# Kernel tuning notes

Hardware: AMD Instinct MI355X
Metric: run time of the kernel (lower is better)

Reference implementation:

```python
import jax, jax.numpy as jnp
import numpy as np

N = 100000
NEG_SLOPE = 0.2
ALPHA = 0.5


def _glorot(key, shape):
    fan_in, fan_out = shape[0], shape[-1]
    lim = jnp.sqrt(6.0 / (fan_in + fan_out))
    return jax.random.uniform(key, shape, jnp.float32, -lim, lim)


def setup_inputs() -> dict:
    key = jax.random.key(0)
    ks = jax.random.split(key, 16)
    x = jax.random.normal(ks[0], (N, 512), jnp.float32)
    spatial_edge_index = jax.random.randint(ks[1], (2, 800000), 0, N, jnp.int64)
    gene_sim_edge_index = jax.random.randint(ks[2], (2, 800000), 0, N, jnp.int64)
    # spatial GAT params (in=512 -> hid=256)
    W_sp = _glorot(ks[3], (512, 256)); a_src_sp = _glorot(ks[4], (256,)); a_dst_sp = _glorot(ks[5], (256,)); b_sp = jnp.zeros((256,), jnp.float32)
    # gene-sim GAT params
    W_gs = _glorot(ks[6], (512, 256)); a_src_gs = _glorot(ks[7], (256,)); a_dst_gs = _glorot(ks[8], (256,)); b_gs = jnp.zeros((256,), jnp.float32)
    # fusion GAT params (hid=256 -> out=64)
    W_fu = _glorot(ks[9], (256, 64)); a_src_fu = _glorot(ks[10], (64,)); a_dst_fu = _glorot(ks[11], (64,)); b_fu = jnp.zeros((64,), jnp.float32)
    return {"x": x, "spatial_edge_index": spatial_edge_index, "gene_sim_edge_index": gene_sim_edge_index,
            "W_sp": W_sp, "a_src_sp": a_src_sp, "a_dst_sp": a_dst_sp, "b_sp": b_sp,
            "W_gs": W_gs, "a_src_gs": a_src_gs, "a_dst_gs": a_dst_gs, "b_gs": b_gs,
            "W_fu": W_fu, "a_src_fu": a_src_fu, "a_dst_fu": a_dst_fu, "b_fu": b_fu}


def gat_conv(x, edge_index, W, a_src, a_dst, bias):
    """PyG GATConv, heads=1, concat=False, add_self_loops=True."""
    n = x.shape[0]
    h = x @ W  # [N, H]
    loops = jnp.arange(n, dtype=edge_index.dtype)
    src = jnp.concatenate([edge_index[0], loops])  # message source j
    dst = jnp.concatenate([edge_index[1], loops])  # aggregation target i
    e = jax.nn.leaky_relu((h @ a_src)[src] + (h @ a_dst)[dst], NEG_SLOPE)  # [E+N]
    # segment softmax over incoming edges of each dst node
    m = jax.ops.segment_max(e, dst, num_segments=n)
    ex = jnp.exp(e - m[dst])
    denom = jax.ops.segment_sum(ex, dst, num_segments=n)
    coef = ex / denom[dst]
    out = jax.ops.segment_sum(coef[:, None] * h[src], dst, num_segments=n)
    return out + bias


def reference(x, spatial_edge_index, gene_sim_edge_index,
              W_sp, a_src_sp, a_dst_sp, b_sp,
              W_gs, a_src_gs, a_dst_gs, b_gs,
              W_fu, a_src_fu, a_dst_fu, b_fu):
    h_spatial = jax.nn.elu(gat_conv(x, spatial_edge_index, W_sp, a_src_sp, a_dst_sp, b_sp))
    h_gene = jax.nn.elu(gat_conv(x, gene_sim_edge_index, W_gs, a_src_gs, a_dst_gs, b_gs))
    h_fused = ALPHA * h_gene + (1.0 - ALPHA) * h_spatial
    return gat_conv(h_fused, spatial_edge_index, W_fu, a_src_fu, a_dst_fu, b_fu)
```

## Files before the change

### kernel.cpp

```cpp
#include <hip/hip_runtime.h>
#include <math.h>


#define NEG_SLOPE 0.2f

typedef __attribute__((ext_vector_type(8))) short bf16x8;
typedef __attribute__((ext_vector_type(4))) float f32x4;
typedef __attribute__((ext_vector_type(2))) float f32x2;

__device__ __forceinline__ unsigned short f2bf(float f) {
  unsigned int u = __float_as_uint(f);
  u = (u + 0x7FFFu + ((u >> 16) & 1u)) >> 16;
  return (unsigned short)u;
}
__device__ __forceinline__ float bf2f(unsigned short u) {
  return __uint_as_float((unsigned int)u << 16);
}
__device__ __forceinline__ f32x2 unpk(unsigned int u) {
  f32x2 r;
  r.x = __uint_as_float(u << 16);
  r.y = __uint_as_float(u & 0xFFFF0000u);
  return r;
}
__device__ __forceinline__ int rl_i(int v, int l) {
  return __builtin_amdgcn_readlane(v, l);
}
__device__ __forceinline__ float rl_f(float v, int l) {
  return __uint_as_float(__builtin_amdgcn_readlane(__float_as_uint(v), l));
}

#define GLOAD16(g, l)                                                   \
  __builtin_amdgcn_global_load_lds(                                     \
      (const __attribute__((address_space(1))) void*)(g),               \
      (__attribute__((address_space(3))) void*)(l), 16, 0, 0)

__global__ __launch_bounds__(256) void wt_bf16_all(const float* __restrict__ W_sp,
                                                   const float* __restrict__ W_gs,
                                                   const float* __restrict__ W_fu,
                                                   unsigned short* __restrict__ wt_sp,
                                                   unsigned short* __restrict__ wt_gs,
                                                   unsigned short* __restrict__ wt_fu) {
  const int i = blockIdx.x * 256 + threadIdx.x;
  if (i < 131072) {
    const int k = i >> 8, n = i & 255;
    wt_sp[n * 512 + k] = f2bf(W_sp[i]);
  } else if (i < 262144) {
    const int j = i - 131072;
    const int k = j >> 8, n = j & 255;
    wt_gs[n * 512 + k] = f2bf(W_gs[j]);
  } else if (i < 278528) {
    const int j = i - 262144;
    const int k = j >> 6, n = j & 63;
    wt_fu[n * 256 + k] = f2bf(W_fu[j]);
  }
}

__global__ __launch_bounds__(256) void hist2(const int* __restrict__ dst_sp,
                                             const int* __restrict__ dst_gs,
                                             int* __restrict__ deg_sp,
                                             int* __restrict__ deg_gs,
                                             int* __restrict__ ord_sp,
                                             int* __restrict__ ord_gs, int E) {
  const int m = blockIdx.x * 256 + threadIdx.x;
  if (m < E) {
    ord_sp[m] = atomicAdd(&deg_sp[dst_sp[m]], 1);
    ord_gs[m] = atomicAdd(&deg_gs[dst_gs[m]], 1);
  }
}

__global__ __launch_bounds__(256) void scan1_2(const int* __restrict__ deg_sp,
                                               const int* __restrict__ deg_gs,
                                               int* __restrict__ rs_sp,
                                               int* __restrict__ rs_gs,
                                               int* __restrict__ parts2, int N) {
  __shared__ int sm[256];
  const int* deg = blockIdx.y ? deg_gs : deg_sp;
  int* rs = blockIdx.y ? rs_gs : rs_sp;
  int* parts = parts2 + blockIdx.y * 512;
  const int i = blockIdx.x * 256 + threadIdx.x;
  const int v = (i < N) ? deg[i] : 0;
  sm[threadIdx.x] = v;
  __syncthreads();
  for (int off = 1; off < 256; off <<= 1) {
    const int x = (threadIdx.x >= off) ? sm[threadIdx.x - off] : 0;
    __syncthreads();
    sm[threadIdx.x] += x;
    __syncthreads();
  }
  if (i < N) rs[i] = sm[threadIdx.x] - v;
  if (threadIdx.x == 255) parts[blockIdx.x] = sm[255];
}

__global__ __launch_bounds__(512) void scan2_2(int* __restrict__ parts2, int nb) {
  __shared__ int sm[512];
  int* parts = parts2 + blockIdx.x * 512;
  const int t = threadIdx.x;
  const int v = (t < nb) ? parts[t] : 0;
  sm[t] = v;
  __syncthreads();
  for (int off = 1; off < 512; off <<= 1) {
    const int x = (t >= off) ? sm[t - off] : 0;
    __syncthreads();
    sm[t] += x;
    __syncthreads();
  }
  if (t < nb) parts[t] = sm[t] - v;
}

__global__ __launch_bounds__(256) void scan3_2(int* __restrict__ rs_sp,
                                               int* __restrict__ rs_gs,
                                               const int* __restrict__ parts2,
                                               int N, int E) {
  int* rs = blockIdx.y ? rs_gs : rs_sp;
  const int* parts = parts2 + blockIdx.y * 512;
  const int i = blockIdx.x * 256 + threadIdx.x;
  if (i < N) rs[i] += parts[blockIdx.x];
  if (i == 0) rs[N] = E;
}

__global__ __launch_bounds__(256) void scatter2(const int* __restrict__ ei_sp,
                                                const int* __restrict__ ei_gs,
                                                const int* __restrict__ rs_sp,
                                                const int* __restrict__ rs_gs,
                                                const int* __restrict__ ord_sp,
                                                const int* __restrict__ ord_gs,
                                                int* __restrict__ csr_sp,
                                                int* __restrict__ csr_gs, int E) {
  const int m = blockIdx.x * 256 + threadIdx.x;
  if (m >= E) return;
  csr_sp[rs_sp[ei_sp[E + m]] + ord_sp[m]] = ei_sp[m];
  csr_gs[rs_gs[ei_gs[E + m]] + ord_gs[m]] = ei_gs[m];
}

__global__ __launch_bounds__(512) void gemm2_fused(const float* __restrict__ x,
                                                   const unsigned short* __restrict__ wsp,
                                                   const unsigned short* __restrict__ wgs,
                                                   unsigned short* __restrict__ hb_sp,
                                                   unsigned short* __restrict__ hb_gs,
                                                   int M) {
  __shared__ unsigned short sA[64 * 64];
  __shared__ unsigned short sW[2][256 * 64];
  const int tid = threadIdx.x;
  const int w = tid >> 6, l = tid & 63;
  const int whalf = w >> 2;
  const int wq = w & 3;
  const int bm = blockIdx.x * 64;

  const int arow0 = tid >> 4;
  const int acol4 = (tid & 15) * 4;
  const unsigned short* __restrict__ wtp = whalf ? wgs : wsp;
  const int wrow_in_ch = l >> 3;
  const int wbyte = ((l & 7) * 16) ^ ((wrow_in_ch & 7) << 4);

  f32x4 acc[4][4] = {};
  for (int k0 = 0; k0 < 512; k0 += 64) {
    __syncthreads();
#pragma unroll
    for (int r = 0; r < 2; ++r) {
      const int row = arow0 + r * 32;
      int grow = bm + row;
      grow = grow < M ? grow : M - 1;
      const float4 v = *(const float4*)(x + (size_t)grow * 512 + k0 + acol4);
      ushort4 o;
      o.x = f2bf(v.x); o.y = f2bf(v.y); o.z = f2bf(v.z); o.w = f2bf(v.w);
      const int byte = (row * 128 + acol4 * 2) ^ ((row & 7) << 4);
      *(ushort4*)(((char*)sA) + byte) = o;
    }
#pragma unroll
    for (int c = 0; c < 8; ++c) {
      const int ch = c * 4 + wq;
      const int grow = ch * 8 + wrow_in_ch;
      const char* g = (const char*)wtp + (size_t)grow * 1024 + (size_t)k0 * 2 + wbyte;
      GLOAD16(g, ((char*)sW[whalf]) + ch * 1024);
    }
    __syncthreads();
#pragma unroll
    for (int ks = 0; ks < 2; ++ks) {
      const int cb = ks * 64 + (l >> 4) * 16;
      bf16x8 af[4], bf[4];
#pragma unroll
      for (int m = 0; m < 4; ++m) {
        const int r = m * 16 + (l & 15);
        af[m] = *(const bf16x8*)(((const char*)sA) + r * 128 + (cb ^ ((r & 7) << 4)));
      }
#pragma unroll
      for (int n = 0; n < 4; ++n) {
        const int r = wq * 64 + n * 16 + (l & 15);
        bf[n] = *(const bf16x8*)(((const char*)sW[whalf]) + r * 128 + (cb ^ ((r & 7) << 4)));
      }
#pragma unroll
      for (int m = 0; m < 4; ++m)
#pragma unroll
        for (int n = 0; n < 4; ++n)
          acc[m][n] = __builtin_amdgcn_mfma_f32_16x16x32_bf16(af[m], bf[n], acc[m][n], 0, 0, 0);
    }
  }
  unsigned short* __restrict__ outp = whalf ? hb_gs : hb_sp;
#pragma unroll
  for (int m = 0; m < 4; ++m) {
#pragma unroll
    for (int r = 0; r < 4; ++r) {
      const int row = bm + m * 16 + (l >> 4) * 4 + r;
      if (row < M) {
#pragma unroll
        for (int n = 0; n < 4; ++n)
          outp[(size_t)row * 256 + wq * 64 + n * 16 + (l & 15)] = f2bf(acc[m][n][r]);
      }
    }
  }
}

__global__ __launch_bounds__(256) void alpha2_256(const ushort4* __restrict__ hsp,
                                                  const ushort4* __restrict__ hgs,
                                                  const float* __restrict__ av_sp_s,
                                                  const float* __restrict__ av_sp_d,
                                                  const float* __restrict__ av_gs_s,
                                                  const float* __restrict__ av_gs_d,
                                                  float* __restrict__ asrc_sp,
                                                  float* __restrict__ adst_sp,
                                                  float* __restrict__ asrc_gs,
                                                  float* __restrict__ adst_gs, int N) {
  const int wave = (int)((blockIdx.x * (size_t)blockDim.x + threadIdx.x) >> 6);
  const int lane = threadIdx.x & 63;
  if (wave >= N) return;
  const ushort4 h1 = hsp[(size_t)wave * 64 + lane];
  const ushort4 h2 = hgs[(size_t)wave * 64 + lane];
  const float4 s1 = ((const float4*)av_sp_s)[lane];
  const float4 d1 = ((const float4*)av_sp_d)[lane];
  const float4 s2 = ((const float4*)av_gs_s)[lane];
  const float4 d2 = ((const float4*)av_gs_d)[lane];
  const float a0 = bf2f(h1.x), a1 = bf2f(h1.y), a2 = bf2f(h1.z), a3 = bf2f(h1.w);
  const float b0 = bf2f(h2.x), b1 = bf2f(h2.y), b2 = bf2f(h2.z), b3 = bf2f(h2.w);
  float p0 = a0 * s1.x + a1 * s1.y + a2 * s1.z + a3 * s1.w;
  float p1 = a0 * d1.x + a1 * d1.y + a2 * d1.z + a3 * d1.w;
  float p2 = b0 * s2.x + b1 * s2.y + b2 * s2.z + b3 * s2.w;
  float p3 = b0 * d2.x + b1 * d2.y + b2 * d2.z + b3 * d2.w;
#pragma unroll
  for (int off = 32; off; off >>= 1) {
    p0 += __shfl_down(p0, off);
    p1 += __shfl_down(p1, off);
    p2 += __shfl_down(p2, off);
    p3 += __shfl_down(p3, off);
  }
  if (lane == 0) {
    asrc_sp[wave] = p0; adst_sp[wave] = p1;
    asrc_gs[wave] = p2; adst_gs[wave] = p3;
  }
}

__global__ __launch_bounds__(256) void gemm_fu_alpha(const unsigned short* __restrict__ A,
                                                     const unsigned short* __restrict__ Bt,
                                                     const float* __restrict__ avs,
                                                     const float* __restrict__ avd,
                                                     unsigned short* __restrict__ C,
                                                     float* __restrict__ asrc,
                                                     float* __restrict__ adst,
                                                     int M) {
  constexpr int K = 256, Nc = 64;
  __shared__ unsigned short sA[128 * 64];
  __shared__ unsigned short sB[64 * 64];
  const int tid = threadIdx.x;
  const int w = tid >> 6, l = tid & 63;
  const int bm = blockIdx.x * 128;
  const int crow = l >> 3;
  const int cbyte = (l & 7) * 16;

  f32x4 acc[2][4] = {};
  for (int k0 = 0; k0 < K; k0 += 64) {
    __syncthreads();
#pragma unroll
    for (int c = 0; c < 4; ++c) {
      const int ch = w * 4 + c;
      int row = bm + ch * 8 + crow;
      row = row < M ? row : M - 1;
      const char* g = (const char*)A + (size_t)row * K * 2 + (size_t)k0 * 2 + cbyte;
      GLOAD16(g, ((char*)sA) + ch * 1024);
    }
#pragma unroll
    for (int c = 0; c < 2; ++c) {
      const int ch = w * 2 + c;
      const int row = ch * 8 + crow;
      const char* g = (const char*)Bt + (size_t)row * K * 2 + (size_t)k0 * 2 + cbyte;
      GLOAD16(g, ((char*)sB) + ch * 1024);
    }
    __syncthreads();
#pragma unroll
    for (int ks = 0; ks < 2; ++ks) {
      bf16x8 af[2], bfr[4];
#pragma unroll
      for (int m = 0; m < 2; ++m) {
        const int r = w * 32 + m * 16 + (l & 15);
        af[m] = *(const bf16x8*)&sA[r * 64 + ks * 32 + (l >> 4) * 8];
      }
#pragma unroll
      for (int n = 0; n < 4; ++n) {
        const int r = n * 16 + (l & 15);
        bfr[n] = *(const bf16x8*)&sB[r * 64 + ks * 32 + (l >> 4) * 8];
      }
#pragma unroll
      for (int m = 0; m < 2; ++m)
#pragma unroll
        for (int n = 0; n < 4; ++n)
          acc[m][n] = __builtin_amdgcn_mfma_f32_16x16x32_bf16(af[m], bfr[n], acc[m][n], 0, 0, 0);
    }
  }
  float as_v[4], ad_v[4];
#pragma unroll
  for (int n = 0; n < 4; ++n) {
    as_v[n] = avs[n * 16 + (l & 15)];
    ad_v[n] = avd[n * 16 + (l & 15)];
  }
#pragma unroll
  for (int m = 0; m < 2; ++m) {
#pragma unroll
    for (int r = 0; r < 4; ++r) {
      const int row = bm + w * 32 + m * 16 + (l >> 4) * 4 + r;
      if (row < M) {
#pragma unroll
        for (int n = 0; n < 4; ++n)
          C[(size_t)row * Nc + n * 16 + (l & 15)] = f2bf(acc[m][n][r]);
      }
      float ps = acc[m][0][r] * as_v[0] + acc[m][1][r] * as_v[1] +
                 acc[m][2][r] * as_v[2] + acc[m][3][r] * as_v[3];
      float pd = acc[m][0][r] * ad_v[0] + acc[m][1][r] * ad_v[1] +
                 acc[m][2][r] * ad_v[2] + acc[m][3][r] * ad_v[3];
#pragma unroll
      for (int off = 1; off < 16; off <<= 1) {
        ps += __shfl_xor(ps, off);
        pd += __shfl_xor(pd, off);
      }
      if ((l & 15) == 0 && row < M) {
        asrc[row] = ps;
        adst[row] = pd;
      }
    }
  }
}

__global__ __launch_bounds__(256) void agg2_blend(const int* __restrict__ rs_sp,
                                                  const int* __restrict__ csr_sp,
                                                  const int* __restrict__ rs_gs,
                                                  const int* __restrict__ csr_gs,
                                                  const float* __restrict__ asrc_sp,
                                                  const float* __restrict__ adst_sp,
                                                  const float* __restrict__ asrc_gs,
                                                  const float* __restrict__ adst_gs,
                                                  const uint2* __restrict__ hsp4,
                                                  const uint2* __restrict__ hgs4,
                                                  const float* __restrict__ b_sp,
                                                  const float* __restrict__ b_gs,
                                                  ushort4* __restrict__ out16, int N) {
  const int d = (int)((blockIdx.x * (size_t)blockDim.x + threadIdx.x) >> 6);
  const int lane = threadIdx.x & 63;
  if (d >= N) return;

  float v_sp[4], v_gs[4];
#pragma unroll
  for (int g = 0; g < 2; ++g) {
    const int* __restrict__ rs   = g ? rs_gs : rs_sp;
    const int* __restrict__ csr  = g ? csr_gs : csr_sp;
    const float* __restrict__ as = g ? asrc_gs : asrc_sp;
    const float* __restrict__ adp = g ? adst_gs : adst_sp;
    const uint2* __restrict__ h4 = g ? hgs4 : hsp4;
    const float* __restrict__ bias = g ? b_gs : b_sp;
    float* __restrict__ vout = g ? v_gs : v_sp;

    const float ad = adp[d];
    float e = as[d] + ad;
    e = e > 0.f ? e : NEG_SLOPE * e;
    const float wself = expf(e);
    float denl = (lane == 0) ? wself : 0.f;
    const uint2 hv = h4[(size_t)d * 64 + lane];
    f32x2 axy = unpk(hv.x) * wself;
    f32x2 azw = unpk(hv.y) * wself;

    const int base = rs[d], mend = rs[d + 1];
    for (int c = base; c < mend; c += 64) {
      const int m = c + lane;
      int s = 0;
      float w = 0.f;
      if (m < mend) {
        s = csr[m];
        float e2 = as[s] + ad;
        e2 = e2 > 0.f ? e2 : NEG_SLOPE * e2;
        w = expf(e2);
      }
      denl += w;
      const int cnt = min(64, mend - c);
      int j = 0;
      for (; j + 3 < cnt; j += 4) {
        const int s0 = rl_i(s, j), s1 = rl_i(s, j + 1), s2 = rl_i(s, j + 2), s3 = rl_i(s, j + 3);
        const float w0 = rl_f(w, j), w1 = rl_f(w, j + 1), w2 = rl_f(w, j + 2), w3 = rl_f(w, j + 3);
        const uint2 a0 = h4[(size_t)s0 * 64 + lane];
        const uint2 a1 = h4[(size_t)s1 * 64 + lane];
        const uint2 a2 = h4[(size_t)s2 * 64 + lane];
        const uint2 a3 = h4[(size_t)s3 * 64 + lane];
        axy += unpk(a0.x) * w0;  azw += unpk(a0.y) * w0;
        axy += unpk(a1.x) * w1;  azw += unpk(a1.y) * w1;
        axy += unpk(a2.x) * w2;  azw += unpk(a2.y) * w2;
        axy += unpk(a3.x) * w3;  azw += unpk(a3.y) * w3;
      }
      for (; j < cnt; ++j) {
        const int sj = rl_i(s, j);
        const float wj = rl_f(w, j);
        const uint2 aj = h4[(size_t)sj * 64 + lane];
        axy += unpk(aj.x) * wj;
        azw += unpk(aj.y) * wj;
      }
    }
#pragma unroll
    for (int off = 32; off; off >>= 1) denl += __shfl_xor(denl, off);
    const float inv = 1.f / denl;
    const float4 b4 = ((const float4*)bias)[lane];
    vout[0] = axy.x * inv + b4.x;
    vout[1] = axy.y * inv + b4.y;
    vout[2] = azw.x * inv + b4.z;
    vout[3] = azw.y * inv + b4.w;
#pragma unroll
    for (int j2 = 0; j2 < 4; ++j2)
      vout[j2] = vout[j2] > 0.f ? vout[j2] : (expf(vout[j2]) - 1.f);
  }

  ushort4 pk;
  pk.x = f2bf(0.5f * v_gs[0] + 0.5f * v_sp[0]);
  pk.y = f2bf(0.5f * v_gs[1] + 0.5f * v_sp[1]);
  pk.z = f2bf(0.5f * v_gs[2] + 0.5f * v_sp[2]);
  pk.w = f2bf(0.5f * v_gs[3] + 0.5f * v_sp[3]);
  out16[(size_t)d * 64 + lane] = pk;
}

__global__ __launch_bounds__(256) void agg_csr64(const int* __restrict__ rs,
                                                 const int* __restrict__ csr,
                                                 const float* __restrict__ asrc,
                                                 const float* __restrict__ adst,
                                                 const unsigned short* __restrict__ h,
                                                 const float* __restrict__ bias,
                                                 float* __restrict__ outb, int N) {
  const int d = (int)((blockIdx.x * (size_t)blockDim.x + threadIdx.x) >> 6);
  const int lane = threadIdx.x & 63;
  if (d >= N) return;
  const float ad = adst[d];

  float e = asrc[d] + ad;
  e = e > 0.f ? e : NEG_SLOPE * e;
  const float wself = expf(e);
  float denl = (lane == 0) ? wself : 0.f;
  f32x2 acc2;
  acc2.x = wself * bf2f(h[(size_t)d * 64 + lane]);
  acc2.y = 0.f;

  const int base = rs[d], mend = rs[d + 1];
  for (int c = base; c < mend; c += 64) {
    const int m = c + lane;
    int s = 0;
    float w = 0.f;
    if (m < mend) {
      s = csr[m];
      float e2 = asrc[s] + ad;
      e2 = e2 > 0.f ? e2 : NEG_SLOPE * e2;
      w = expf(e2);
    }
    denl += w;
    const int cnt = min(64, mend - c);
    int j = 0;
    for (; j + 3 < cnt; j += 4) {
      const int s0 = rl_i(s, j), s1 = rl_i(s, j + 1), s2 = rl_i(s, j + 2), s3 = rl_i(s, j + 3);
      const float w0 = rl_f(w, j), w1 = rl_f(w, j + 1), w2 = rl_f(w, j + 2), w3 = rl_f(w, j + 3);
      f32x2 h01, h23, w01, w23;
      h01.x = bf2f(h[(size_t)s0 * 64 + lane]);
      h01.y = bf2f(h[(size_t)s1 * 64 + lane]);
      h23.x = bf2f(h[(size_t)s2 * 64 + lane]);
      h23.y = bf2f(h[(size_t)s3 * 64 + lane]);
      w01.x = w0; w01.y = w1;
      w23.x = w2; w23.y = w3;
      acc2 += h01 * w01;
      acc2 += h23 * w23;
    }
    for (; j < cnt; ++j) {
      const int sj = rl_i(s, j);
      const float wj = rl_f(w, j);
      acc2.x += wj * bf2f(h[(size_t)sj * 64 + lane]);
    }
  }
  float acc = acc2.x + acc2.y;
#pragma unroll
  for (int off = 32; off; off >>= 1) denl += __shfl_xor(denl, off);
  outb[(size_t)d * 64 + lane] = acc / denl + bias[lane];
}

extern "C" void kernel_launch(void* const* d_in, const int* in_sizes, int n_in,
                              void* d_out, int out_size, void* d_ws, size_t ws_size,
                              hipStream_t stream) {
  const float* x        = (const float*)d_in[0];
  const int*   ei_sp    = (const int*)d_in[1];
  const int*   ei_gs    = (const int*)d_in[2];
  const float* W_sp     = (const float*)d_in[3];
  const float* a_src_sp = (const float*)d_in[4];
  const float* a_dst_sp = (const float*)d_in[5];
  const float* b_sp     = (const float*)d_in[6];
  const float* W_gs     = (const float*)d_in[7];
  const float* a_src_gs = (const float*)d_in[8];
  const float* a_dst_gs = (const float*)d_in[9];
  const float* b_gs     = (const float*)d_in[10];
  const float* W_fu     = (const float*)d_in[11];
  const float* a_src_fu = (const float*)d_in[12];
  const float* a_dst_fu = (const float*)d_in[13];
  const float* b_fu     = (const float*)d_in[14];
  float* out = (float*)d_out;

  const int N = in_sizes[0] / 512;
  const int E = in_sizes[1] / 2;
  const int nb = (N + 255) / 256;

  unsigned short* wt_sp = (unsigned short*)d_ws;
  unsigned short* wt_gs = wt_sp + 256 * 512;
  unsigned short* wt_fu = wt_gs + 256 * 512;
  unsigned short* hb_sp = wt_fu + 64 * 256;
  unsigned short* hb_gs = hb_sp + (size_t)N * 256;
  unsigned short* hfb   = hb_gs + (size_t)N * 256;
  unsigned short* hfu   = hfb + (size_t)N * 256;
  float* asrc_sp = (float*)(hfu + (size_t)N * 64);
  float* adst_sp = asrc_sp + N;
  float* asrc_gs = adst_sp + N;
  float* adst_gs = asrc_gs + N;
  int* rs_sp  = (int*)(adst_gs + N);
  int* rs_gs  = rs_sp + (N + 1);
  int* csr_sp = rs_gs + (N + 1);
  int* csr_gs = csr_sp + E;
  int* deg_sp = csr_gs + E;
  int* deg_gs = deg_sp + N;
  int* parts2 = deg_gs + N;
  int* ord_sp = parts2 + 1024;
  int* ord_gs = ord_sp + E;

  const int BLK = 256;
  const int eGrid = (E + BLK - 1) / BLK;
  const int nodeWaveGrid = (N + 3) / 4;

  hipMemsetAsync(deg_sp, 0, (size_t)2 * N * 4, stream);
  hist2<<<eGrid, BLK, 0, stream>>>(ei_sp + E, ei_gs + E, deg_sp, deg_gs,
                                   ord_sp, ord_gs, E);
  scan1_2<<<dim3(nb, 2), BLK, 0, stream>>>(deg_sp, deg_gs, rs_sp, rs_gs, parts2, N);
  scan2_2<<<2, 512, 0, stream>>>(parts2, nb);
  scan3_2<<<dim3(nb, 2), BLK, 0, stream>>>(rs_sp, rs_gs, parts2, N, E);
  scatter2<<<eGrid, BLK, 0, stream>>>(ei_sp, ei_gs, rs_sp, rs_gs, ord_sp, ord_gs,
                                      csr_sp, csr_gs, E);

  wt_bf16_all<<<(278528 + 255) / 256, BLK, 0, stream>>>(W_sp, W_gs, W_fu,
                                                        wt_sp, wt_gs, wt_fu);

  gemm2_fused<<<(N + 63) / 64, 512, 0, stream>>>(x, wt_sp, wt_gs, hb_sp, hb_gs, N);

  alpha2_256<<<nodeWaveGrid, BLK, 0, stream>>>((const ushort4*)hb_sp,
                                               (const ushort4*)hb_gs,
                                               a_src_sp, a_dst_sp, a_src_gs, a_dst_gs,
                                               asrc_sp, adst_sp, asrc_gs, adst_gs, N);

  agg2_blend<<<nodeWaveGrid, BLK, 0, stream>>>(rs_sp, csr_sp, rs_gs, csr_gs,
                                               asrc_sp, adst_sp, asrc_gs, adst_gs,
                                               (const uint2*)hb_sp,
                                               (const uint2*)hb_gs,
                                               b_sp, b_gs, (ushort4*)hfb, N);

  gemm_fu_alpha<<<(N + 127) / 128, BLK, 0, stream>>>(hfb, wt_fu, a_src_fu, a_dst_fu,
                                                     hfu, asrc_sp, adst_sp, N);
  agg_csr64<<<nodeWaveGrid, BLK, 0, stream>>>(rs_sp, csr_sp, asrc_sp, adst_sp,
                                              hfu, b_fu, out, N);
}
```

Baseline: 467.0 us.

## Co-schedule edge histogram with GEMM and CSR scatter with alpha kernel

Merges the independent edge-degree histogram into the dual-projection GEMM launch as extra blocks, and the CSR scatter into the attention-logit kernel, using a block-index split. This removes two kernel launches and lets the latency-bound atomic and scatter work overlap with the compute- and bandwidth-bound kernels. The histogram blocks are launched at 512 threads and carry the GEMM's shared-memory footprint, which can reduce occupancy for those blocks. The weight conversion kernel is moved ahead of the memset.

Result: faster. 451.8 us (median of 2 runs) (-3.3%).

```diff
diff --git a/kernel.cpp b/kernel.cpp
--- a/kernel.cpp
+++ b/kernel.cpp
@@ -55,19 +55,6 @@
   }
 }
 
-__global__ __launch_bounds__(256) void hist2(const int* __restrict__ dst_sp,
-                                             const int* __restrict__ dst_gs,
-                                             int* __restrict__ deg_sp,
-                                             int* __restrict__ deg_gs,
-                                             int* __restrict__ ord_sp,
-                                             int* __restrict__ ord_gs, int E) {
-  const int m = blockIdx.x * 256 + threadIdx.x;
-  if (m < E) {
-    ord_sp[m] = atomicAdd(&deg_sp[dst_sp[m]], 1);
-    ord_gs[m] = atomicAdd(&deg_gs[dst_gs[m]], 1);
-  }
-}
-
 __global__ __launch_bounds__(256) void scan1_2(const int* __restrict__ deg_sp,
                                                const int* __restrict__ deg_gs,
                                                int* __restrict__ rs_sp,
@@ -118,33 +105,33 @@
   if (i == 0) rs[N] = E;
 }
 
-__global__ __launch_bounds__(256) void scatter2(const int* __restrict__ ei_sp,
-                                                const int* __restrict__ ei_gs,
-                                                const int* __restrict__ rs_sp,
-                                                const int* __restrict__ rs_gs,
-                                                const int* __restrict__ ord_sp,
-                                                const int* __restrict__ ord_gs,
-                                                int* __restrict__ csr_sp,
-                                                int* __restrict__ csr_gs, int E) {
-  const int m = blockIdx.x * 256 + threadIdx.x;
-  if (m >= E) return;
-  csr_sp[rs_sp[ei_sp[E + m]] + ord_sp[m]] = ei_sp[m];
-  csr_gs[rs_gs[ei_gs[E + m]] + ord_gs[m]] = ei_gs[m];
-}
-
-__global__ __launch_bounds__(512) void gemm2_fused(const float* __restrict__ x,
-                                                   const unsigned short* __restrict__ wsp,
-                                                   const unsigned short* __restrict__ wgs,
-                                                   unsigned short* __restrict__ hb_sp,
-                                                   unsigned short* __restrict__ hb_gs,
-                                                   int M) {
+__global__ __launch_bounds__(512) void gemm2_hist(const float* __restrict__ x,
+                                                  const unsigned short* __restrict__ wsp,
+                                                  const unsigned short* __restrict__ wgs,
+                                                  unsigned short* __restrict__ hb_sp,
+                                                  unsigned short* __restrict__ hb_gs,
+                                                  const int* __restrict__ dst_sp,
+                                                  const int* __restrict__ dst_gs,
+                                                  int* __restrict__ deg_sp,
+                                                  int* __restrict__ deg_gs,
+                                                  int* __restrict__ ord_sp,
+                                                  int* __restrict__ ord_gs,
+                                                  int nHist, int E, int M) {
+  if ((int)blockIdx.x < nHist) {
+    const int m = blockIdx.x * 512 + threadIdx.x;
+    if (m < E) {
+      ord_sp[m] = atomicAdd(&deg_sp[dst_sp[m]], 1);
+      ord_gs[m] = atomicAdd(&deg_gs[dst_gs[m]], 1);
+    }
+    return;
+  }
   __shared__ unsigned short sA[64 * 64];
   __shared__ unsigned short sW[2][256 * 64];
   const int tid = threadIdx.x;
   const int w = tid >> 6, l = tid & 63;
   const int whalf = w >> 2;
   const int wq = w & 3;
-  const int bm = blockIdx.x * 64;
+  const int bm = (blockIdx.x - nHist) * 64;
 
   const int arow0 = tid >> 4;
   const int acol4 = (tid & 15) * 4;
@@ -210,17 +197,34 @@
   }
 }
 
-__global__ __launch_bounds__(256) void alpha2_256(const ushort4* __restrict__ hsp,
-                                                  const ushort4* __restrict__ hgs,
-                                                  const float* __restrict__ av_sp_s,
-                                                  const float* __restrict__ av_sp_d,
-                                                  const float* __restrict__ av_gs_s,
-                                                  const float* __restrict__ av_gs_d,
-                                                  float* __restrict__ asrc_sp,
-                                                  float* __restrict__ adst_sp,
-                                                  float* __restrict__ asrc_gs,
-                                                  float* __restrict__ adst_gs, int N) {
-  const int wave = (int)((blockIdx.x * (size_t)blockDim.x + threadIdx.x) >> 6);
+__global__ __launch_bounds__(256) void alpha_scatter(const ushort4* __restrict__ hsp,
+                                                     const ushort4* __restrict__ hgs,
+                                                     const float* __restrict__ av_sp_s,
+                                                     const float* __restrict__ av_sp_d,
+                                                     const float* __restrict__ av_gs_s,
+                                                     const float* __restrict__ av_gs_d,
+                                                     float* __restrict__ asrc_sp,
+                                                     float* __restrict__ adst_sp,
+                                                     float* __restrict__ asrc_gs,
+                                                     float* __restrict__ adst_gs,
+                                                     const int* __restrict__ ei_sp,
+                                                     const int* __restrict__ ei_gs,
+                                                     const int* __restrict__ rs_sp,
+                                                     const int* __restrict__ rs_gs,
+                                                     const int* __restrict__ ord_sp,
+                                                     const int* __restrict__ ord_gs,
+                                                     int* __restrict__ csr_sp,
+                                                     int* __restrict__ csr_gs,
+                                                     int nScat, int E, int N) {
+  if ((int)blockIdx.x < nScat) {
+    const int m = blockIdx.x * 256 + threadIdx.x;
+    if (m < E) {
+      csr_sp[rs_sp[ei_sp[E + m]] + ord_sp[m]] = ei_sp[m];
+      csr_gs[rs_gs[ei_gs[E + m]] + ord_gs[m]] = ei_gs[m];
+    }
+    return;
+  }
+  const int wave = (int)(((blockIdx.x - nScat) * (size_t)256 + threadIdx.x) >> 6);
   const int lane = threadIdx.x & 63;
   if (wave >= N) return;
   const ushort4 h1 = hsp[(size_t)wave * 64 + lane];
@@ -534,27 +538,30 @@
   int* ord_gs = ord_sp + E;
 
   const int BLK = 256;
-  const int eGrid = (E + BLK - 1) / BLK;
   const int nodeWaveGrid = (N + 3) / 4;
-
+  const int nHist = (E + 511) / 512;
+  const int nGemm = (N + 63) / 64;
+  const int nScat = (E + 255) / 256;
+
+  wt_bf16_all<<<(278528 + 255) / 256, BLK, 0, stream>>>(W_sp, W_gs, W_fu,
+                                                        wt_sp, wt_gs, wt_fu);
   hipMemsetAsync(deg_sp, 0, (size_t)2 * N * 4, stream);
-  hist2<<<eGrid, BLK, 0, stream>>>(ei_sp + E, ei_gs + E, deg_sp, deg_gs,
-                                   ord_sp, ord_gs, E);
+
+  gemm2_hist<<<nHist + nGemm, 512, 0, stream>>>(x, wt_sp, wt_gs, hb_sp, hb_gs,
+                                                ei_sp + E, ei_gs + E,
+                                                deg_sp, deg_gs, ord_sp, ord_gs,
+                                                nHist, E, N);
+
   scan1_2<<<dim3(nb, 2), BLK, 0, stream>>>(deg_sp, deg_gs, rs_sp, rs_gs, parts2, N);
   scan2_2<<<2, 512, 0, stream>>>(parts2, nb);
   scan3_2<<<dim3(nb, 2), BLK, 0, stream>>>(rs_sp, rs_gs, parts2, N, E);
-  scatter2<<<eGrid, BLK, 0, stream>>>(ei_sp, ei_gs, rs_sp, rs_gs, ord_sp, ord_gs,
-                                      csr_sp, csr_gs, E);
-
-  wt_bf16_all<<<(278528 + 255) / 256, BLK, 0, stream>>>(W_sp, W_gs, W_fu,
-                                                        wt_sp, wt_gs, wt_fu);
-
-  gemm2_fused<<<(N + 63) / 64, 512, 0, stream>>>(x, wt_sp, wt_gs, hb_sp, hb_gs, N);
-
-  alpha2_256<<<nodeWaveGrid, BLK, 0, stream>>>((const ushort4*)hb_sp,
-                                               (const ushort4*)hb_gs,
-                                               a_src_sp, a_dst_sp, a_src_gs, a_dst_gs,
-                                               asrc_sp, adst_sp, asrc_gs, adst_gs, N);
+
+  alpha_scatter<<<nScat + nodeWaveGrid, BLK, 0, stream>>>(
+      (const ushort4*)hb_sp, (const ushort4*)hb_gs,
+      a_src_sp, a_dst_sp, a_src_gs, a_dst_gs,
+      asrc_sp, adst_sp, asrc_gs, adst_gs,
+      ei_sp, ei_gs, rs_sp, rs_gs, ord_sp, ord_gs,
+      csr_sp, csr_gs, nScat, E, N);
 
   agg2_blend<<<nodeWaveGrid, BLK, 0, stream>>>(rs_sp, csr_sp, rs_gs, csr_gs,
                                                asrc_sp, adst_sp, asrc_gs, adst_gs,
```
